# Kernel tuning notes

Hardware: AMD Instinct MI355X
Metric: run time of the kernel (lower is better)

Reference implementation:

```python
import jax, jax.numpy as jnp
import numpy as np

B, A, D, H = 2048, 16, 128, 512

def setup_inputs() -> dict:
    key = jax.random.key(0)
    k0, k1, k2, k3, k4 = jax.random.split(key, 5)
    s1 = 1.0 / np.sqrt(D)
    s2 = 1.0 / np.sqrt(H)
    return {
        "attribute_embeddings": jax.random.normal(k0, (B, A, D), dtype=jnp.float32),
        "W1": jax.random.uniform(k1, (H, D), jnp.float32, -s1, s1),  # torch Linear weight [out,in]
        "b1": jax.random.uniform(k2, (H,), jnp.float32, -s1, s1),
        "W2": jax.random.uniform(k3, (D, H), jnp.float32, -s2, s2),
        "b2": jax.random.uniform(k4, (D,), jnp.float32, -s2, s2),
    }

def reference(attribute_embeddings, W1, b1, W2, b2):
    x = attribute_embeddings  # [B, A, D]
    # all pairwise elementwise products: [B, A, A, D]
    pairs = x[:, :, None, :] * x[:, None, :, :]
    # shared 2-layer MLP applied to every pair (torch Linear: y = x @ W.T + b)
    h = jax.nn.relu(jnp.einsum("bijd,hd->bijh", pairs, W1) + b1)
    inter = jnp.einsum("bijh,dh->bijd", h, W2) + b2  # [B, A, A, D]
    # sum over first attribute index i -> [B, A, D]
    return jnp.sum(inter, axis=1)
```

## Files before the change

### kernel.cpp

```cpp
#include <hip/hip_runtime.h>


#define BATCH 2048
#define AA 16
#define DD 128
#define HH 512

typedef __bf16 bf16;
typedef bf16  bf16x4 __attribute__((ext_vector_type(4)));
typedef bf16  bf16x8 __attribute__((ext_vector_type(8)));
typedef float f32x4  __attribute__((ext_vector_type(4)));

__device__ inline f32x4 splat4(float v) { f32x4 r = {v, v, v, v}; return r; }

__global__ __launch_bounds__(256, 1)
void convert_weights(const float* __restrict__ W1,
                     const float* __restrict__ W2,
                     bf16* __restrict__ wsb)
{
    int t = blockIdx.x * 256 + threadIdx.x;
    f32x4 v = (t < 16384) ? *(const f32x4*)(W1 + 4 * t)
                          : *(const f32x4*)(W2 + 4 * (t - 16384));
    bf16x4 o;
    o[0] = (bf16)v[0]; o[1] = (bf16)v[1]; o[2] = (bf16)v[2]; o[3] = (bf16)v[3];
    *(bf16x4*)(wsb + 4 * t) = o;
}

__global__ __launch_bounds__(256, 2)
void interact_kernel(const float* __restrict__ x,
                     const bf16*  __restrict__ W1b,
                     const float* __restrict__ b1,
                     const bf16*  __restrict__ W2b,
                     const float* __restrict__ b2,
                     float* __restrict__ out)
{
    __shared__ bf16 xs[16][136];
    __shared__ bf16 ps[2][16][136];
    __shared__ bf16 hs[16][520];

    const int b    = blockIdx.x;
    const int tid  = threadIdx.x;
    const int wave = tid >> 6;
    const int lane = tid & 63;
    const int quad = lane >> 4;
    const int col  = lane & 15;

    const int jrow = tid >> 4;
    const int d0   = (tid & 15) * 8;

    {
        const float* src = x + (size_t)b * (AA * DD) + jrow * DD + d0;
        f32x4 lo = *(const f32x4*)src;
        f32x4 hi = *(const f32x4*)(src + 4);
        bf16x8 v;
        v[0] = (bf16)lo[0]; v[1] = (bf16)lo[1]; v[2] = (bf16)lo[2]; v[3] = (bf16)lo[3];
        v[4] = (bf16)hi[0]; v[5] = (bf16)hi[1]; v[6] = (bf16)hi[2]; v[7] = (bf16)hi[3];
        *(bf16x8*)(&xs[jrow][d0]) = v;
    }

    bf16x8 w1f[8][4];
    float  b1f[8];
#pragma unroll
    for (int n = 0; n < 8; ++n) {
        int h  = wave * 128 + n * 16 + col;
        b1f[n] = b1[h];
#pragma unroll
        for (int kk = 0; kk < 4; ++kk)
            w1f[n][kk] = *(const bf16x8*)(W1b + h * DD + kk * 32 + quad * 8);
    }

    f32x4 hsum[8];
#pragma unroll
    for (int n = 0; n < 8; ++n) hsum[n] = splat4(0.f);

    __syncthreads();

    float xjf[8];
    {
        bf16x8 xj = *(bf16x8*)(&xs[jrow][d0]);
#pragma unroll
        for (int e = 0; e < 8; ++e) xjf[e] = (float)xj[e];
    }

    for (int i = 0; i < 16; ++i) {
        const int p = i & 1;

        {
            bf16x8 xi = *(bf16x8*)(&xs[i][d0]);
            bf16x8 pr;
#pragma unroll
            for (int e = 0; e < 8; ++e)
                pr[e] = (bf16)(xjf[e] * (float)xi[e]);
            *(bf16x8*)(&ps[p][jrow][d0]) = pr;
        }
        __syncthreads();

        bf16x8 af[4];
#pragma unroll
        for (int kk = 0; kk < 4; ++kk)
            af[kk] = *(bf16x8*)(&ps[p][col][kk * 32 + quad * 8]);

        f32x4 acc[8];
#pragma unroll
        for (int n = 0; n < 8; ++n)
            acc[n] = __builtin_amdgcn_mfma_f32_16x16x32_bf16(
                af[0], w1f[n][0], splat4(b1f[n]), 0, 0, 0);
#pragma unroll
        for (int kk = 1; kk < 4; ++kk)
#pragma unroll
            for (int n = 0; n < 8; ++n)
                acc[n] = __builtin_amdgcn_mfma_f32_16x16x32_bf16(
                    af[kk], w1f[n][kk], acc[n], 0, 0, 0);

#pragma unroll
        for (int n = 0; n < 8; ++n)
#pragma unroll
            for (int r = 0; r < 4; ++r)
                hsum[n][r] += fmaxf(acc[n][r], 0.f);
    }

#pragma unroll
    for (int n = 0; n < 8; ++n)
#pragma unroll
        for (int r = 0; r < 4; ++r)
            hs[quad * 4 + r][wave * 128 + n * 16 + col] = (bf16)hsum[n][r];

    __syncthreads();

    f32x4 acc2[2];
#pragma unroll
    for (int n2 = 0; n2 < 2; ++n2)
        acc2[n2] = splat4(16.f * b2[wave * 32 + n2 * 16 + col]);

#pragma unroll
    for (int ks = 0; ks < 16; ++ks) {
        int h0 = ks * 32 + quad * 8;
        bf16x8 a2 = *(bf16x8*)(&hs[col][h0]);
#pragma unroll
        for (int n2 = 0; n2 < 2; ++n2) {
            int d = wave * 32 + n2 * 16 + col;
            bf16x8 bw = *(const bf16x8*)(W2b + d * HH + h0);
            acc2[n2] = __builtin_amdgcn_mfma_f32_16x16x32_bf16(
                a2, bw, acc2[n2], 0, 0, 0);
        }
    }

#pragma unroll
    for (int n2 = 0; n2 < 2; ++n2)
#pragma unroll
        for (int r = 0; r < 4; ++r) {
            int j = quad * 4 + r;
            int d = wave * 32 + n2 * 16 + col;
            out[(size_t)b * (AA * DD) + j * DD + d] = acc2[n2][r];
        }
}

extern "C" void kernel_launch(void* const* d_in, const int* in_sizes, int n_in,
                              void* d_out, int out_size, void* d_ws, size_t ws_size,
                              hipStream_t stream)
{
    const float* x  = (const float*)d_in[0];
    const float* W1 = (const float*)d_in[1];
    const float* b1 = (const float*)d_in[2];
    const float* W2 = (const float*)d_in[3];
    const float* b2 = (const float*)d_in[4];
    float* out = (float*)d_out;

    bf16* wsb = (bf16*)d_ws;
    convert_weights<<<128, 256, 0, stream>>>(W1, W2, wsb);

    const bf16* W1b = wsb;
    const bf16* W2b = wsb + (size_t)HH * DD;
    interact_kernel<<<BATCH, 256, 0, stream>>>(x, W1b, b1, W2b, b2, out);
}
```

Before: 147.7 us.

## Precompute all pair products into shared memory and software-pipeline A-fragment loads

Instead of forming one pair-product tile per i with a barrier each iteration, all 16 product tiles are written to shared memory up front with a single barrier. The GEMM loop then double-buffers A fragments in registers, loading the next tile while the MFMAs for the current one run. x is kept in fp32 in shared memory and registers, so products are computed from unrounded inputs. The hidden-sum buffer aliases the product buffer, and an extra barrier before reuse keeps that safe. Shared memory use grows, which may lower occupancy below two blocks per CU, and register pressure rises from the extra fragment buffer.

```diff
diff --git a/kernel.cpp b/kernel.cpp
--- a/kernel.cpp
+++ b/kernel.cpp
@@ -34,9 +34,10 @@
                      const float* __restrict__ b2,
                      float* __restrict__ out)
 {
-    __shared__ bf16 xs[16][136];
-    __shared__ bf16 ps[2][16][136];
-    __shared__ bf16 hs[16][520];
+    __shared__ float xs[16][136];
+    __shared__ __align__(16) unsigned char smem_raw[16 * 16 * 136 * 2];
+    bf16 (*ps)[16][136] = reinterpret_cast<bf16(*)[16][136]>(smem_raw);
+    bf16 (*hs)[520]     = reinterpret_cast<bf16(*)[520]>(smem_raw);
 
     const int b    = blockIdx.x;
     const int tid  = threadIdx.x;
@@ -48,14 +49,13 @@
     const int jrow = tid >> 4;
     const int d0   = (tid & 15) * 8;
 
+    f32x4 xlo, xhi;
     {
         const float* src = x + (size_t)b * (AA * DD) + jrow * DD + d0;
-        f32x4 lo = *(const f32x4*)src;
-        f32x4 hi = *(const f32x4*)(src + 4);
-        bf16x8 v;
-        v[0] = (bf16)lo[0]; v[1] = (bf16)lo[1]; v[2] = (bf16)lo[2]; v[3] = (bf16)lo[3];
-        v[4] = (bf16)hi[0]; v[5] = (bf16)hi[1]; v[6] = (bf16)hi[2]; v[7] = (bf16)hi[3];
-        *(bf16x8*)(&xs[jrow][d0]) = v;
+        xlo = *(const f32x4*)src;
+        xhi = *(const f32x4*)(src + 4);
+        *(f32x4*)(&xs[jrow][d0])     = xlo;
+        *(f32x4*)(&xs[jrow][d0 + 4]) = xhi;
     }
 
     bf16x8 w1f[8][4];
@@ -75,49 +75,72 @@
 
     __syncthreads();
 
-    float xjf[8];
-    {
-        bf16x8 xj = *(bf16x8*)(&xs[jrow][d0]);
+#pragma unroll 4
+    for (int i = 0; i < 16; ++i) {
+        f32x4 alo = *(f32x4*)(&xs[i][d0]);
+        f32x4 ahi = *(f32x4*)(&xs[i][d0 + 4]);
+        bf16x8 pr;
 #pragma unroll
-        for (int e = 0; e < 8; ++e) xjf[e] = (float)xj[e];
+        for (int e = 0; e < 4; ++e) pr[e]     = (bf16)(alo[e] * xlo[e]);
+#pragma unroll
+        for (int e = 0; e < 4; ++e) pr[4 + e] = (bf16)(ahi[e] * xhi[e]);
+        *(bf16x8*)(&ps[i][jrow][d0]) = pr;
     }
+    __syncthreads();
 
-    for (int i = 0; i < 16; ++i) {
-        const int p = i & 1;
+    bf16x8 afA[4], afB[4];
+#pragma unroll
+    for (int kk = 0; kk < 4; ++kk)
+        afA[kk] = *(bf16x8*)(&ps[0][col][kk * 32 + quad * 8]);
 
-        {
-            bf16x8 xi = *(bf16x8*)(&xs[i][d0]);
-            bf16x8 pr;
-#pragma unroll
-            for (int e = 0; e < 8; ++e)
-                pr[e] = (bf16)(xjf[e] * (float)xi[e]);
-            *(bf16x8*)(&ps[p][jrow][d0]) = pr;
-        }
-        __syncthreads();
-
-        bf16x8 af[4];
+    for (int i = 0; i < 16; i += 2) {
 #pragma unroll
         for (int kk = 0; kk < 4; ++kk)
-            af[kk] = *(bf16x8*)(&ps[p][col][kk * 32 + quad * 8]);
-
-        f32x4 acc[8];
-#pragma unroll
-        for (int n = 0; n < 8; ++n)
-            acc[n] = __builtin_amdgcn_mfma_f32_16x16x32_bf16(
-                af[0], w1f[n][0], splat4(b1f[n]), 0, 0, 0);
-#pragma unroll
-        for (int kk = 1; kk < 4; ++kk)
+            afB[kk] = *(bf16x8*)(&ps[i + 1][col][kk * 32 + quad * 8]);
+        {
+            f32x4 acc[8];
 #pragma unroll
             for (int n = 0; n < 8; ++n)
                 acc[n] = __builtin_amdgcn_mfma_f32_16x16x32_bf16(
-                    af[kk], w1f[n][kk], acc[n], 0, 0, 0);
+                    afA[0], w1f[n][0], splat4(b1f[n]), 0, 0, 0);
+#pragma unroll
+            for (int kk = 1; kk < 4; ++kk)
+#pragma unroll
+                for (int n = 0; n < 8; ++n)
+                    acc[n] = __builtin_amdgcn_mfma_f32_16x16x32_bf16(
+                        afA[kk], w1f[n][kk], acc[n], 0, 0, 0);
+#pragma unroll
+            for (int n = 0; n < 8; ++n)
+#pragma unroll
+                for (int r = 0; r < 4; ++r)
+                    hsum[n][r] += fmaxf(acc[n][r], 0.f);
+        }
 
+        const int inext = (i + 2) & 15;
 #pragma unroll
-        for (int n = 0; n < 8; ++n)
+        for (int kk = 0; kk < 4; ++kk)
+            afA[kk] = *(bf16x8*)(&ps[inext][col][kk * 32 + quad * 8]);
+        {
+            f32x4 acc[8];
 #pragma unroll
-            for (int r = 0; r < 4; ++r)
-                hsum[n][r] += fmaxf(acc[n][r], 0.f);
+            for (int n = 0; n < 8; ++n)
+                acc[n] = __builtin_amdgcn_mfma_f32_16x16x32_bf16(
+                    afB[0], w1f[n][0], splat4(b1f[n]), 0, 0, 0);
+#pragma unroll
+            for (int kk = 1; kk < 4; ++kk)
+#pragma unroll
+                for (int n = 0; n < 8; ++n)
+                    acc[n] = __builtin_amdgcn_mfma_f32_16x16x32_bf16(
+                        afB[kk], w1f[n][kk], acc[n], 0, 0, 0);
+#pragma unroll
+            for (int n = 0; n < 8; ++n)
+#pragma unroll
+                for (int r = 0; r < 4; ++r)
+                    hsum[n][r] += fmaxf(acc[n][r], 0.f);
+        }
     }
+
+    __syncthreads();
 
 #pragma unroll
     for (int n = 0; n < 8; ++n)
```

After: 194.9 us. 1.32x slower.

## Use 512 threads per block and precompute all pair products before MFMA loop

Applied to the files above, without the earlier changes.

Doubles the block to 8 waves so each wave owns 64 hidden units and 16 output columns, halving the W1 fragments held in registers. All 16 pairwise products are written to LDS up front, which removes the per-iteration barrier, and the hs buffer aliases the ps buffer. x is kept in fp32 in LDS. The intent is lower register pressure, more waves in flight to hide latency, and fewer syncs. The cost is more LDS per block (about 78KB), which may limit how many blocks fit per CU.

```diff
diff --git a/kernel.cpp b/kernel.cpp
--- a/kernel.cpp
+++ b/kernel.cpp
@@ -26,7 +26,7 @@
     *(bf16x4*)(wsb + 4 * t) = o;
 }
 
-__global__ __launch_bounds__(256, 2)
+__global__ __launch_bounds__(512, 4)
 void interact_kernel(const float* __restrict__ x,
                      const bf16*  __restrict__ W1b,
                      const float* __restrict__ b1,
@@ -34,9 +34,10 @@
                      const float* __restrict__ b2,
                      float* __restrict__ out)
 {
-    __shared__ bf16 xs[16][136];
-    __shared__ bf16 ps[2][16][136];
-    __shared__ bf16 hs[16][520];
+    __shared__ float xs[16][136];
+    __shared__ __align__(16) unsigned char smem_raw[16 * 16 * 136 * 2];
+    bf16 (*ps)[16][136] = reinterpret_cast<bf16(*)[16][136]>(smem_raw);
+    bf16 (*hs)[520]     = reinterpret_cast<bf16(*)[520]>(smem_raw);
 
     const int b    = blockIdx.x;
     const int tid  = threadIdx.x;
@@ -45,114 +46,95 @@
     const int quad = lane >> 4;
     const int col  = lane & 15;
 
-    const int jrow = tid >> 4;
-    const int d0   = (tid & 15) * 8;
+    const int jrow = tid >> 5;
+    const int dq   = (tid & 31) * 4;
 
+    f32x4 xj;
     {
-        const float* src = x + (size_t)b * (AA * DD) + jrow * DD + d0;
-        f32x4 lo = *(const f32x4*)src;
-        f32x4 hi = *(const f32x4*)(src + 4);
-        bf16x8 v;
-        v[0] = (bf16)lo[0]; v[1] = (bf16)lo[1]; v[2] = (bf16)lo[2]; v[3] = (bf16)lo[3];
-        v[4] = (bf16)hi[0]; v[5] = (bf16)hi[1]; v[6] = (bf16)hi[2]; v[7] = (bf16)hi[3];
-        *(bf16x8*)(&xs[jrow][d0]) = v;
+        const float* src = x + (size_t)b * (AA * DD) + jrow * DD + dq;
+        xj = *(const f32x4*)src;
+        *(f32x4*)(&xs[jrow][dq]) = xj;
     }
 
-    bf16x8 w1f[8][4];
-    float  b1f[8];
+    bf16x8 w1f[4][4];
+    float  b1f[4];
 #pragma unroll
-    for (int n = 0; n < 8; ++n) {
-        int h  = wave * 128 + n * 16 + col;
+    for (int n = 0; n < 4; ++n) {
+        int h  = wave * 64 + n * 16 + col;
         b1f[n] = b1[h];
 #pragma unroll
         for (int kk = 0; kk < 4; ++kk)
             w1f[n][kk] = *(const bf16x8*)(W1b + h * DD + kk * 32 + quad * 8);
     }
 
-    f32x4 hsum[8];
+    f32x4 hsum[4];
 #pragma unroll
-    for (int n = 0; n < 8; ++n) hsum[n] = splat4(0.f);
+    for (int n = 0; n < 4; ++n) hsum[n] = splat4(0.f);
 
     __syncthreads();
 
-    float xjf[8];
-    {
-        bf16x8 xj = *(bf16x8*)(&xs[jrow][d0]);
+#pragma unroll 4
+    for (int i = 0; i < 16; ++i) {
+        f32x4 xi = *(f32x4*)(&xs[i][dq]);
+        bf16x4 pr;
 #pragma unroll
-        for (int e = 0; e < 8; ++e) xjf[e] = (float)xj[e];
+        for (int e = 0; e < 4; ++e) pr[e] = (bf16)(xj[e] * xi[e]);
+        *(bf16x4*)(&ps[i][jrow][dq]) = pr;
     }
+    __syncthreads();
 
+#pragma unroll 1
     for (int i = 0; i < 16; ++i) {
-        const int p = i & 1;
-
-        {
-            bf16x8 xi = *(bf16x8*)(&xs[i][d0]);
-            bf16x8 pr;
-#pragma unroll
-            for (int e = 0; e < 8; ++e)
-                pr[e] = (bf16)(xjf[e] * (float)xi[e]);
-            *(bf16x8*)(&ps[p][jrow][d0]) = pr;
-        }
-        __syncthreads();
-
         bf16x8 af[4];
 #pragma unroll
         for (int kk = 0; kk < 4; ++kk)
-            af[kk] = *(bf16x8*)(&ps[p][col][kk * 32 + quad * 8]);
+            af[kk] = *(bf16x8*)(&ps[i][col][kk * 32 + quad * 8]);
 
-        f32x4 acc[8];
+        f32x4 acc[4];
 #pragma unroll
-        for (int n = 0; n < 8; ++n)
+        for (int n = 0; n < 4; ++n)
             acc[n] = __builtin_amdgcn_mfma_f32_16x16x32_bf16(
                 af[0], w1f[n][0], splat4(b1f[n]), 0, 0, 0);
 #pragma unroll
         for (int kk = 1; kk < 4; ++kk)
 #pragma unroll
-            for (int n = 0; n < 8; ++n)
+            for (int n = 0; n < 4; ++n)
                 acc[n] = __builtin_amdgcn_mfma_f32_16x16x32_bf16(
                     af[kk], w1f[n][kk], acc[n], 0, 0, 0);
 
 #pragma unroll
-        for (int n = 0; n < 8; ++n)
+        for (int n = 0; n < 4; ++n)
 #pragma unroll
             for (int r = 0; r < 4; ++r)
                 hsum[n][r] += fmaxf(acc[n][r], 0.f);
     }
 
+    __syncthreads();
+
 #pragma unroll
-    for (int n = 0; n < 8; ++n)
+    for (int n = 0; n < 4; ++n)
 #pragma unroll
         for (int r = 0; r < 4; ++r)
-            hs[quad * 4 + r][wave * 128 + n * 16 + col] = (bf16)hsum[n][r];
+            hs[quad * 4 + r][wave * 64 + n * 16 + col] = (bf16)hsum[n][r];
 
     __syncthreads();
 
-    f32x4 acc2[2];
-#pragma unroll
-    for (int n2 = 0; n2 < 2; ++n2)
-        acc2[n2] = splat4(16.f * b2[wave * 32 + n2 * 16 + col]);
+    const int d = wave * 16 + col;
+    f32x4 acc2 = splat4(16.f * b2[d]);
 
 #pragma unroll
     for (int ks = 0; ks < 16; ++ks) {
         int h0 = ks * 32 + quad * 8;
         bf16x8 a2 = *(bf16x8*)(&hs[col][h0]);
-#pragma unroll
-        for (int n2 = 0; n2 < 2; ++n2) {
-            int d = wave * 32 + n2 * 16 + col;
-            bf16x8 bw = *(const bf16x8*)(W2b + d * HH + h0);
-            acc2[n2] = __builtin_amdgcn_mfma_f32_16x16x32_bf16(
-                a2, bw, acc2[n2], 0, 0, 0);
-        }
+        bf16x8 bw = *(const bf16x8*)(W2b + d * HH + h0);
+        acc2 = __builtin_amdgcn_mfma_f32_16x16x32_bf16(a2, bw, acc2, 0, 0, 0);
     }
 
 #pragma unroll
-    for (int n2 = 0; n2 < 2; ++n2)
-#pragma unroll
-        for (int r = 0; r < 4; ++r) {
-            int j = quad * 4 + r;
-            int d = wave * 32 + n2 * 16 + col;
-            out[(size_t)b * (AA * DD) + j * DD + d] = acc2[n2][r];
-        }
+    for (int r = 0; r < 4; ++r) {
+        int j = quad * 4 + r;
+        out[(size_t)b * (AA * DD) + j * DD + d] = acc2[r];
+    }
 }
 
 extern "C" void kernel_launch(void* const* d_in, const int* in_sizes, int n_in,
@@ -171,5 +153,5 @@
 
     const bf16* W1b = wsb;
     const bf16* W2b = wsb + (size_t)HH * DD;
-    interact_kernel<<<BATCH, 256, 0, stream>>>(x, W1b, b1, W2b, b2, out);
+    interact_kernel<<<BATCH, 512, 0, stream>>>(x, W1b, b1, W2b, b2, out);
 }
```

Measured after the change: 148.1 us. Within noise of the previous version (+0.3%).
